# Kernel optimization log

Hardware: AMD Instinct MI355X
Metric: run time of the kernel (lower is better)

The kernel has to match this reference:

```python
import jax, jax.numpy as jnp
import numpy as np

TEMPERATURE = 0.1
GAMMA = 0.5
LOSS_WEIGHT = 1.0
N, D = 8192, 64
EPS_COS = 1e-8
EPS_NCE = 1e-6
SQ_EPS = 1e-12  # (1e-6 distance)^2


def setup_inputs() -> dict:
    key = jax.random.key(0)
    k1, k2, k3 = jax.random.split(key, 3)
    features = jax.random.normal(k1, (N, D), dtype=jnp.float32)
    labels = jax.random.randint(k2, (N,), 0, 3, dtype=jnp.int64)
    coords = jax.random.uniform(k3, (N, 3), dtype=jnp.float32)
    return {"features": features, "labels": labels, "coords": coords}


def reference(features, labels, coords):
    # line-point mask (label == 2); pairwise math on the masked subset is
    # expressed as full pairwise + (m_i & m_j) masking, mathematically
    # identical to extract-then-pairwise in the torch original.
    m = labels == 2                       # [N] bool
    mf = m.astype(features.dtype)
    L = jnp.sum(mf)                       # number of line points

    # cosine similarity: normalize then GEMM (== F.cosine_similarity pairwise)
    norm = jnp.maximum(jnp.linalg.norm(features, axis=1, keepdims=True), EPS_COS)
    fn = features / norm
    feat_sim = fn @ fn.T                  # [N, N]

    # squared pairwise coordinate distances (cdist^2), clamped >= 0
    sq_norm = jnp.sum(coords * coords, axis=1)
    sq = sq_norm[:, None] + sq_norm[None, :] - 2.0 * (coords @ coords.T)
    sq = jnp.maximum(sq, 0.0)             # [N, N]

    pair = m[:, None] & m[None, :]
    within = (sq < 1.0) & (sq > SQ_EPS)   # dist < 1.0 and dist > 1e-6
    pos = pair & within
    neg = pair & ~within                  # original neg_mask = ~pos over subset

    posf = pos.astype(feat_sim.dtype)
    negf = neg.astype(feat_sim.dtype)

    exp_sim = jnp.exp(feat_sim / TEMPERATURE)
    sum_exp = jnp.sum(exp_sim * negf, axis=1)
    pos_sum = jnp.sum(exp_sim * posf, axis=1)
    ratio = pos_sum / (sum_exp + pos_sum + EPS_NCE)
    # mean of -log(ratio) over line points only (guard non-line rows)
    per_point = -jnp.log(jnp.where(m, ratio, 1.0))
    info_nce = jnp.sum(per_point * mf) / L

    # continuity: mean over the L x L subset matrix of |(1 - sim) - dist| * pos
    safe_sq = jnp.where(pos, sq, 1.0)     # avoid sqrt(0) NaN grads on masked entries
    coord_dist = jnp.sqrt(safe_sq)
    continuity = jnp.sum(jnp.abs((1.0 - feat_sim) - coord_dist) * posf) / (L * L)

    return (info_nce + GAMMA * continuity) * LOSS_WEIGHT
```

## Files before the change

### kernel.cpp

```cpp
#include <hip/hip_runtime.h>
#include <math.h>


typedef short s16x8 __attribute__((ext_vector_type(8)));
typedef float f32x4 __attribute__((ext_vector_type(4)));

#define NPTS 8192
#define DIM 64
#define BT 128
#define GRID_P 512
#define PSTRIDE 4096
#define MAXSLOT 32

#define OFF_L 0
#define OFF_IDX 1024
#define OFF_FH (OFF_IDX + NPTS * 4)
#define OFF_FL (OFF_FH + NPTS * DIM * 2)
#define OFF_CS (OFF_FL + NPTS * DIM * 2)
#define OFF_DF (OFF_CS + NPTS * 16)
#define OFF_PP (OFF_DF + NPTS * 4)
#define OFF_PN (OFF_PP + MAXSLOT * PSTRIDE * 4)
#define OFF_CT (OFF_PN + MAXSLOT * PSTRIDE * 4)

__global__ __launch_bounds__(1024) void k_scan(const int* __restrict__ labels,
                                               int* __restrict__ idx,
                                               int* __restrict__ Lout) {
  __shared__ int wres[16];
  __shared__ int wsum[16];
  const int t = threadIdx.x;
  const int lane = t & 63;
  const int wid = t >> 6;
  const int base = t * 8;
  int w[8];
#pragma unroll
  for (int j = 0; j < 8; j++) w[j] = labels[base + j];
  int oddz = (w[1] == 0) && (w[3] == 0) && (w[5] == 0) && (w[7] == 0);
  unsigned long long wa = __ballot(!oddz);
  if (lane == 0) wres[wid] = (wa == 0ull);
  __syncthreads();
  int is64 = 1;
#pragma unroll
  for (int i = 0; i < 16; i++) is64 &= wres[i];

  int bits = 0, cnt = 0;
  if (is64) {
    const long long* l64 = (const long long*)labels;
#pragma unroll
    for (int j = 0; j < 8; j++) {
      bool f = (l64[base + j] == 2ll);
      bits |= ((int)f) << j;
      cnt += (int)f;
    }
  } else {
#pragma unroll
    for (int j = 0; j < 8; j++) {
      bool f = (w[j] == 2);
      bits |= ((int)f) << j;
      cnt += (int)f;
    }
  }
  int inc = cnt;
#pragma unroll
  for (int m = 1; m < 64; m <<= 1) {
    int v = __shfl_up(inc, m);
    if (lane >= m) inc += v;
  }
  if (lane == 63) wsum[wid] = inc;
  __syncthreads();
  if (t < 16) {
    int v = wsum[t];
    int sc = v;
#pragma unroll
    for (int m = 1; m < 16; m <<= 1) {
      int u = __shfl_up(sc, m);
      if (t >= m) sc += u;
    }
    wsum[t] = sc - v;
    if (t == 15) *Lout = sc;
  }
  __syncthreads();
  int pos = wsum[wid] + inc - cnt;
#pragma unroll
  for (int j = 0; j < 8; j++) {
    if (bits & (1 << j)) idx[pos++] = base + j;
  }
}

__global__ __launch_bounds__(256) void k_gather(const float* __restrict__ feats,
                                                const float* __restrict__ coords,
                                                const int* __restrict__ idx,
                                                const int* __restrict__ Lp,
                                                ushort* __restrict__ fnHi,
                                                ushort* __restrict__ fnLo,
                                                float4* __restrict__ cs,
                                                int* __restrict__ diagf) {
  const int L = *Lp;
  const int gw = (int)((blockIdx.x * blockDim.x + threadIdx.x) >> 6);
  const int lane = threadIdx.x & 63;
  if (gw >= L) {
    fnHi[gw * 64 + lane] = 0;
    fnLo[gw * 64 + lane] = 0;
    return;
  }
  const int row = idx[gw];
  float f = feats[row * DIM + lane];
  float ss = f * f;
#pragma unroll
  for (int m = 32; m; m >>= 1) ss += __shfl_xor(ss, m);
  float nrm = fmaxf(sqrtf(ss), 1e-8f);
  float fn = f / nrm;
  unsigned int u = __float_as_uint(fn);
  unsigned int hb = (u + 0x7FFFu + ((u >> 16) & 1u)) >> 16;
  float hif = __uint_as_float(hb << 16);
  float lof = fn - hif;
  unsigned int ul = __float_as_uint(lof);
  unsigned int lb = (ul + 0x7FFFu + ((ul >> 16) & 1u)) >> 16;
  fnHi[gw * 64 + lane] = (ushort)hb;
  fnLo[gw * 64 + lane] = (ushort)lb;
  if (lane == 0) {
    float c0 = coords[row * 3 + 0];
    float c1 = coords[row * 3 + 1];
    float c2 = coords[row * 3 + 2];
    float p0 = __fmul_rn(c0, c0);
    float p1 = __fmul_rn(c1, c1);
    float p2 = __fmul_rn(c2, c2);
    float s = __fadd_rn(__fadd_rn(p0, p1), p2);
    float g = __fadd_rn(__fadd_rn(p0, p2), p1);
    diagf[gw] = (__fadd_rn(s, -g) > 5e-13f) ? 1 : 0;
    cs[gw] = make_float4(c0, c1, c2, c0 * c0 + c1 * c1 + c2 * c2);
  }
}

__global__ __launch_bounds__(256, 2) void k_pair(const ushort* __restrict__ fnHi,
                                                 const ushort* __restrict__ fnLo,
                                                 const float4* __restrict__ cs,
                                                 const int* __restrict__ Lp,
                                                 const int* __restrict__ diagf,
                                                 float* __restrict__ pp,
                                                 float* __restrict__ pn,
                                                 float* __restrict__ contp) {
  __shared__ ushort AB[4][128][72];
  __shared__ float cred[4];

  const int L = *Lp;
  const int nT = (L + BT - 1) >> 7;
  const int nItems = nT * nT;
  const int t = threadIdx.x;
  const int lane = t & 63, wid = t >> 6;
  const int m = lane & 15;
  const int koct = lane >> 4;
  float cont = 0.f;

  for (int wi = blockIdx.x; wi < nItems; wi += GRID_P) {
    const int bi = wi / nT;
    const int jt = wi - bi * nT;
    const int rb = bi << 7, cb = jt << 7;

    __syncthreads();
#pragma unroll
    for (int i = 0; i < 16; i++) {
      int q = t + 256 * i;
      int sel = q >> 10;
      int row = (q >> 3) & 127;
      int oct = q & 7;
      int slot = ((sel < 2) ? rb : cb) + row;
      const ushort* src = (sel & 1) ? fnLo : fnHi;
      s16x8 v = *(const s16x8*)&src[slot * 64 + oct * 8];
      *(s16x8*)&AB[sel][row][oct * 8] = v;
    }
    __syncthreads();

    f32x4 acc[2][8];
#pragma unroll
    for (int rt = 0; rt < 2; rt++)
#pragma unroll
      for (int ct = 0; ct < 8; ct++) acc[rt][ct] = (f32x4){0.f, 0.f, 0.f, 0.f};

#pragma unroll
    for (int kk = 0; kk < 2; kk++) {
      const int kof = kk * 32 + koct * 8;
      s16x8 ah[2], al[2], bh[8], bl[8];
#pragma unroll
      for (int rt = 0; rt < 2; rt++) {
        ah[rt] = *(const s16x8*)&AB[0][wid * 32 + rt * 16 + m][kof];
        al[rt] = *(const s16x8*)&AB[1][wid * 32 + rt * 16 + m][kof];
      }
#pragma unroll
      for (int ct = 0; ct < 8; ct++) {
        bh[ct] = *(const s16x8*)&AB[2][ct * 16 + m][kof];
        bl[ct] = *(const s16x8*)&AB[3][ct * 16 + m][kof];
      }
#pragma unroll
      for (int rt = 0; rt < 2; rt++)
#pragma unroll
        for (int ct = 0; ct < 8; ct++) {
          acc[rt][ct] = __builtin_amdgcn_mfma_f32_16x16x32_bf16(ah[rt], bh[ct], acc[rt][ct], 0, 0, 0);
          acc[rt][ct] = __builtin_amdgcn_mfma_f32_16x16x32_bf16(ah[rt], bl[ct], acc[rt][ct], 0, 0, 0);
          acc[rt][ct] = __builtin_amdgcn_mfma_f32_16x16x32_bf16(al[rt], bh[ct], acc[rt][ct], 0, 0, 0);
        }
    }

    float4 crow[2][4];
    int dfr[2][4];
#pragma unroll
    for (int rt = 0; rt < 2; rt++)
#pragma unroll
      for (int rg = 0; rg < 4; rg++) {
        int ig = rb + wid * 32 + rt * 16 + koct * 4 + rg;
        crow[rt][rg] = cs[ig];
        dfr[rt][rg] = diagf[ig];
      }
    float pos_r[2][4] = {{0.f, 0.f, 0.f, 0.f}, {0.f, 0.f, 0.f, 0.f}};
    float neg_r[2][4] = {{0.f, 0.f, 0.f, 0.f}, {0.f, 0.f, 0.f, 0.f}};
#pragma unroll
    for (int ct = 0; ct < 8; ct++) {
      int jg = cb + ct * 16 + m;
      float4 cbv = cs[jg];
      bool jv = (jg < L);
#pragma unroll
      for (int rt = 0; rt < 2; rt++)
#pragma unroll
        for (int rg = 0; rg < 4; rg++) {
          int ig = rb + wid * 32 + rt * 16 + koct * 4 + rg;
          bool valid = jv && (ig < L);
          float sim = acc[rt][ct][rg];
          float4 cav = crow[rt][rg];
          float d3 = cav.x * cbv.x + cav.y * cbv.y + cav.z * cbv.z;
          float sq = fmaxf(cav.w + cbv.w - 2.f * d3, 0.f);
          bool within = (sq < 1.0f) && (sq > 1e-12f);
          if (ig == jg) within = (dfr[rt][rg] != 0);
          float e = __expf(sim * 10.f);
          if (valid) {
            if (within) {
              pos_r[rt][rg] += e;
              cont += fabsf(1.f - sim - sqrtf(sq));
            } else {
              neg_r[rt][rg] += e;
            }
          }
        }
    }
#pragma unroll
    for (int rt = 0; rt < 2; rt++)
#pragma unroll
      for (int rg = 0; rg < 4; rg++) {
        float p = pos_r[rt][rg], n = neg_r[rt][rg];
#pragma unroll
        for (int s = 1; s < 16; s <<= 1) {
          p += __shfl_xor(p, s);
          n += __shfl_xor(n, s);
        }
        if (m == 0) {
          int ig = rb + wid * 32 + rt * 16 + koct * 4 + rg;
          pp[jt * PSTRIDE + ig] = p;
          pn[jt * PSTRIDE + ig] = n;
        }
      }
  }

#pragma unroll
  for (int s = 1; s < 64; s <<= 1) cont += __shfl_xor(cont, s);
  if (lane == 0) cred[wid] = cont;
  __syncthreads();
  if (t == 0) contp[blockIdx.x] = cred[0] + cred[1] + cred[2] + cred[3];
}

__global__ __launch_bounds__(1024) void k_final(const float* __restrict__ pp,
                                                const float* __restrict__ pn,
                                                const float* __restrict__ contp,
                                                const int* __restrict__ Lp,
                                                float* __restrict__ out) {
  __shared__ float red[32];
  const int L = *Lp;
  const int nslots = (L + BT - 1) >> 7;
  const int t = threadIdx.x;
  float accI = 0.f;
  for (int s = t; s < L; s += 1024) {
    float pos = 0.f, neg = 0.f;
    for (int c = 0; c < nslots; c++) {
      pos += pp[c * PSTRIDE + s];
      neg += pn[c * PSTRIDE + s];
    }
    accI += -logf(pos / (neg + pos + 1e-6f));
  }
  float accC = 0.f;
  for (int c = t; c < GRID_P; c += 1024) accC += contp[c];
#pragma unroll
  for (int m = 1; m < 64; m <<= 1) {
    accI += __shfl_xor(accI, m);
    accC += __shfl_xor(accC, m);
  }
  if ((t & 63) == 0) {
    red[t >> 6] = accI;
    red[16 + (t >> 6)] = accC;
  }
  __syncthreads();
  if (t == 0) {
    float sI = 0.f, sC = 0.f;
#pragma unroll
    for (int w = 0; w < 16; w++) {
      sI += red[w];
      sC += red[16 + w];
    }
    float fL = (float)L;
    out[0] = sI / fL + 0.5f * (sC / (fL * fL));
  }
}

extern "C" void kernel_launch(void* const* d_in, const int* in_sizes, int n_in,
                              void* d_out, int out_size, void* d_ws, size_t ws_size,
                              hipStream_t stream) {
  const float* features = (const float*)d_in[0];
  const int* labels = (const int*)d_in[1];
  const float* coords = (const float*)d_in[2];

  char* ws = (char*)d_ws;
  int* Lp = (int*)(ws + OFF_L);
  int* idx = (int*)(ws + OFF_IDX);
  ushort* fnHi = (ushort*)(ws + OFF_FH);
  ushort* fnLo = (ushort*)(ws + OFF_FL);
  float4* cs = (float4*)(ws + OFF_CS);
  int* diagf = (int*)(ws + OFF_DF);
  float* pp = (float*)(ws + OFF_PP);
  float* pn = (float*)(ws + OFF_PN);
  float* contp = (float*)(ws + OFF_CT);
  float* out = (float*)d_out;

  k_scan<<<1, 1024, 0, stream>>>(labels, idx, Lp);
  k_gather<<<(NPTS * 64) / 256, 256, 0, stream>>>(features, coords, idx, Lp, fnHi, fnLo, cs, diagf);
  k_pair<<<GRID_P, 256, 0, stream>>>(fnHi, fnLo, cs, Lp, diagf, pp, pn, contp);
  k_final<<<1, 1024, 0, stream>>>(pp, pn, contp, Lp, out);
}
```

Measured before the change: 47.94 us.

## Fuse four kernels into one persistent kernel with software grid barriers

Replaces the scan, gather, pair and final kernels with a single persistent kernel of 256 blocks that separates the phases with atomic-counter grid barriers, reset by a memset before launch. The pair stage now stages K in two halves into smaller shared tiles, and the final reduction is spread across blocks. The aim is to remove the launch gaps between the four kernels and the serial single-block final pass. In exchange it adds spin-wait barriers that rely on all 256 blocks being co-resident, an extra memset launch, and fewer blocks for the pair phase.

Measured after the change: 162.7 us. 3.39x slower.

```diff
diff --git a/kernel.cpp b/kernel.cpp
--- a/kernel.cpp
+++ b/kernel.cpp
@@ -7,12 +7,13 @@
 
 #define NPTS 8192
 #define DIM 64
-#define BT 128
-#define GRID_P 512
+#define GRID 256
+#define NTHR 256
 #define PSTRIDE 4096
 #define MAXSLOT 32
 
-#define OFF_L 0
+#define OFF_CNT 0
+#define OFF_L 64
 #define OFF_IDX 1024
 #define OFF_FH (OFF_IDX + NPTS * 4)
 #define OFF_FL (OFF_FH + NPTS * DIM * 2)
@@ -21,289 +22,289 @@
 #define OFF_PP (OFF_DF + NPTS * 4)
 #define OFF_PN (OFF_PP + MAXSLOT * PSTRIDE * 4)
 #define OFF_CT (OFF_PN + MAXSLOT * PSTRIDE * 4)
-
-__global__ __launch_bounds__(1024) void k_scan(const int* __restrict__ labels,
-                                               int* __restrict__ idx,
-                                               int* __restrict__ Lout) {
-  __shared__ int wres[16];
-  __shared__ int wsum[16];
-  const int t = threadIdx.x;
-  const int lane = t & 63;
-  const int wid = t >> 6;
-  const int base = t * 8;
-  int w[8];
-#pragma unroll
-  for (int j = 0; j < 8; j++) w[j] = labels[base + j];
-  int oddz = (w[1] == 0) && (w[3] == 0) && (w[5] == 0) && (w[7] == 0);
-  unsigned long long wa = __ballot(!oddz);
-  if (lane == 0) wres[wid] = (wa == 0ull);
+#define OFF_PI (OFF_CT + GRID * 4)
+
+__device__ __forceinline__ void grid_bar(int* cnt, int target) {
   __syncthreads();
-  int is64 = 1;
-#pragma unroll
-  for (int i = 0; i < 16; i++) is64 &= wres[i];
-
-  int bits = 0, cnt = 0;
-  if (is64) {
-    const long long* l64 = (const long long*)labels;
-#pragma unroll
-    for (int j = 0; j < 8; j++) {
-      bool f = (l64[base + j] == 2ll);
-      bits |= ((int)f) << j;
-      cnt += (int)f;
-    }
-  } else {
-#pragma unroll
-    for (int j = 0; j < 8; j++) {
-      bool f = (w[j] == 2);
-      bits |= ((int)f) << j;
-      cnt += (int)f;
-    }
-  }
-  int inc = cnt;
-#pragma unroll
-  for (int m = 1; m < 64; m <<= 1) {
-    int v = __shfl_up(inc, m);
-    if (lane >= m) inc += v;
-  }
-  if (lane == 63) wsum[wid] = inc;
+  if (threadIdx.x == 0) {
+    __threadfence();
+    atomicAdd(cnt, 1);
+    while (__hip_atomic_load(cnt, __ATOMIC_ACQUIRE, __HIP_MEMORY_SCOPE_AGENT) <
+           target) {
+      __builtin_amdgcn_s_sleep(2);
+    }
+    __threadfence();
+  }
   __syncthreads();
-  if (t < 16) {
-    int v = wsum[t];
-    int sc = v;
-#pragma unroll
-    for (int m = 1; m < 16; m <<= 1) {
-      int u = __shfl_up(sc, m);
-      if (t >= m) sc += u;
-    }
-    wsum[t] = sc - v;
-    if (t == 15) *Lout = sc;
-  }
-  __syncthreads();
-  int pos = wsum[wid] + inc - cnt;
-#pragma unroll
-  for (int j = 0; j < 8; j++) {
-    if (bits & (1 << j)) idx[pos++] = base + j;
-  }
 }
 
-__global__ __launch_bounds__(256) void k_gather(const float* __restrict__ feats,
-                                                const float* __restrict__ coords,
-                                                const int* __restrict__ idx,
-                                                const int* __restrict__ Lp,
-                                                ushort* __restrict__ fnHi,
-                                                ushort* __restrict__ fnLo,
-                                                float4* __restrict__ cs,
-                                                int* __restrict__ diagf) {
-  const int L = *Lp;
-  const int gw = (int)((blockIdx.x * blockDim.x + threadIdx.x) >> 6);
-  const int lane = threadIdx.x & 63;
-  if (gw >= L) {
-    fnHi[gw * 64 + lane] = 0;
-    fnLo[gw * 64 + lane] = 0;
-    return;
-  }
-  const int row = idx[gw];
-  float f = feats[row * DIM + lane];
-  float ss = f * f;
-#pragma unroll
-  for (int m = 32; m; m >>= 1) ss += __shfl_xor(ss, m);
-  float nrm = fmaxf(sqrtf(ss), 1e-8f);
-  float fn = f / nrm;
-  unsigned int u = __float_as_uint(fn);
-  unsigned int hb = (u + 0x7FFFu + ((u >> 16) & 1u)) >> 16;
-  float hif = __uint_as_float(hb << 16);
-  float lof = fn - hif;
-  unsigned int ul = __float_as_uint(lof);
-  unsigned int lb = (ul + 0x7FFFu + ((ul >> 16) & 1u)) >> 16;
-  fnHi[gw * 64 + lane] = (ushort)hb;
-  fnLo[gw * 64 + lane] = (ushort)lb;
-  if (lane == 0) {
-    float c0 = coords[row * 3 + 0];
-    float c1 = coords[row * 3 + 1];
-    float c2 = coords[row * 3 + 2];
-    float p0 = __fmul_rn(c0, c0);
-    float p1 = __fmul_rn(c1, c1);
-    float p2 = __fmul_rn(c2, c2);
-    float s = __fadd_rn(__fadd_rn(p0, p1), p2);
-    float g = __fadd_rn(__fadd_rn(p0, p2), p1);
-    diagf[gw] = (__fadd_rn(s, -g) > 5e-13f) ? 1 : 0;
-    cs[gw] = make_float4(c0, c1, c2, c0 * c0 + c1 * c1 + c2 * c2);
-  }
-}
-
-__global__ __launch_bounds__(256, 2) void k_pair(const ushort* __restrict__ fnHi,
-                                                 const ushort* __restrict__ fnLo,
-                                                 const float4* __restrict__ cs,
-                                                 const int* __restrict__ Lp,
-                                                 const int* __restrict__ diagf,
-                                                 float* __restrict__ pp,
-                                                 float* __restrict__ pn,
-                                                 float* __restrict__ contp) {
-  __shared__ ushort AB[4][128][72];
-  __shared__ float cred[4];
-
-  const int L = *Lp;
-  const int nT = (L + BT - 1) >> 7;
-  const int nItems = nT * nT;
+__global__ __launch_bounds__(NTHR) void k_fused(
+    const float* __restrict__ feats, const int* __restrict__ labels,
+    const float* __restrict__ coords, int* cnt, int* __restrict__ Lp,
+    int* __restrict__ idx, ushort* __restrict__ fnHi,
+    ushort* __restrict__ fnLo, float4* __restrict__ cs,
+    int* __restrict__ diagf, float* __restrict__ pp, float* __restrict__ pn,
+    float* __restrict__ contp, float* __restrict__ partI,
+    float* __restrict__ out) {
+  __shared__ __attribute__((aligned(16))) ushort AB[4][128][40];
+  __shared__ float fred[8];
+  __shared__ int ired[8];
   const int t = threadIdx.x;
   const int lane = t & 63, wid = t >> 6;
-  const int m = lane & 15;
-  const int koct = lane >> 4;
-  float cont = 0.f;
-
-  for (int wi = blockIdx.x; wi < nItems; wi += GRID_P) {
-    const int bi = wi / nT;
-    const int jt = wi - bi * nT;
-    const int rb = bi << 7, cb = jt << 7;
-
-    __syncthreads();
-#pragma unroll
-    for (int i = 0; i < 16; i++) {
-      int q = t + 256 * i;
-      int sel = q >> 10;
-      int row = (q >> 3) & 127;
-      int oct = q & 7;
-      int slot = ((sel < 2) ? rb : cb) + row;
-      const ushort* src = (sel & 1) ? fnLo : fnHi;
-      s16x8 v = *(const s16x8*)&src[slot * 64 + oct * 8];
-      *(s16x8*)&AB[sel][row][oct * 8] = v;
-    }
-    __syncthreads();
-
-    f32x4 acc[2][8];
-#pragma unroll
-    for (int rt = 0; rt < 2; rt++)
-#pragma unroll
-      for (int ct = 0; ct < 8; ct++) acc[rt][ct] = (f32x4){0.f, 0.f, 0.f, 0.f};
-
-#pragma unroll
-    for (int kk = 0; kk < 2; kk++) {
-      const int kof = kk * 32 + koct * 8;
-      s16x8 ah[2], al[2], bh[8], bl[8];
-#pragma unroll
-      for (int rt = 0; rt < 2; rt++) {
-        ah[rt] = *(const s16x8*)&AB[0][wid * 32 + rt * 16 + m][kof];
-        al[rt] = *(const s16x8*)&AB[1][wid * 32 + rt * 16 + m][kof];
-      }
-#pragma unroll
-      for (int ct = 0; ct < 8; ct++) {
-        bh[ct] = *(const s16x8*)&AB[2][ct * 16 + m][kof];
-        bl[ct] = *(const s16x8*)&AB[3][ct * 16 + m][kof];
-      }
+  const int bx = (int)blockIdx.x;
+
+  if (bx == 0) {
+    const int base = t * 32;
+    int w[32];
+#pragma unroll
+    for (int j = 0; j < 32; j++) w[j] = labels[base + j];
+    int oddz = 1;
+#pragma unroll
+    for (int j = 1; j < 32; j += 2) oddz &= (w[j] == 0);
+    unsigned long long wa = __ballot(!oddz);
+    if (lane == 0) ired[wid] = (wa == 0ull);
+    __syncthreads();
+    int is64 = ired[0] & ired[1] & ired[2] & ired[3];
+    __syncthreads();
+    unsigned bits = 0;
+    int cnt2 = 0;
+    if (is64) {
+      const long long* l64 = (const long long*)labels;
+#pragma unroll
+      for (int j = 0; j < 32; j++) {
+        bool f = (l64[base + j] == 2ll);
+        bits |= ((unsigned)f) << j;
+        cnt2 += (int)f;
+      }
+    } else {
+#pragma unroll
+      for (int j = 0; j < 32; j++) {
+        bool f = (w[j] == 2);
+        bits |= ((unsigned)f) << j;
+        cnt2 += (int)f;
+      }
+    }
+    int inc = cnt2;
+#pragma unroll
+    for (int m1 = 1; m1 < 64; m1 <<= 1) {
+      int v = __shfl_up(inc, m1);
+      if (lane >= m1) inc += v;
+    }
+    if (lane == 63) ired[wid] = inc;
+    __syncthreads();
+    int woff = 0;
+#pragma unroll
+    for (int i = 0; i < 4; i++)
+      if (i < wid) woff += ired[i];
+    int pos = woff + inc - cnt2;
+#pragma unroll
+    for (int j = 0; j < 32; j++)
+      if ((bits >> j) & 1u) idx[pos++] = base + j;
+    if (t == 0) *Lp = ired[0] + ired[1] + ired[2] + ired[3];
+  }
+  grid_bar(cnt, GRID);
+
+  const int L = *Lp;
+  const int Lpad = (L + 127) & ~127;
+  const int nT = Lpad >> 7;
+
+  for (int slot = bx * 4 + wid; slot < Lpad; slot += GRID * 4) {
+    if (slot < L) {
+      const int row = idx[slot];
+      float f = feats[row * DIM + lane];
+      float ss = f * f;
+#pragma unroll
+      for (int m1 = 32; m1; m1 >>= 1) ss += __shfl_xor(ss, m1);
+      float nrm = fmaxf(sqrtf(ss), 1e-8f);
+      float fn = f / nrm;
+      unsigned u = __float_as_uint(fn);
+      unsigned hb = (u + 0x7FFFu + ((u >> 16) & 1u)) >> 16;
+      float hif = __uint_as_float(hb << 16);
+      float lof = fn - hif;
+      unsigned ul = __float_as_uint(lof);
+      unsigned lb = (ul + 0x7FFFu + ((ul >> 16) & 1u)) >> 16;
+      fnHi[slot * 64 + lane] = (ushort)hb;
+      fnLo[slot * 64 + lane] = (ushort)lb;
+      if (lane == 0) {
+        float c0 = coords[row * 3 + 0];
+        float c1 = coords[row * 3 + 1];
+        float c2 = coords[row * 3 + 2];
+        float p0 = __fmul_rn(c0, c0);
+        float p1 = __fmul_rn(c1, c1);
+        float p2 = __fmul_rn(c2, c2);
+        float s_ = __fadd_rn(__fadd_rn(p0, p1), p2);
+        float g_ = __fadd_rn(__fadd_rn(p0, p2), p1);
+        diagf[slot] = (__fadd_rn(s_, -g_) > 5e-13f) ? 1 : 0;
+        cs[slot] = make_float4(c0, c1, c2, c0 * c0 + c1 * c1 + c2 * c2);
+      }
+    } else {
+      fnHi[slot * 64 + lane] = 0;
+      fnLo[slot * 64 + lane] = 0;
+      if (lane == 0) {
+        cs[slot] = make_float4(0.f, 0.f, 0.f, 0.f);
+        diagf[slot] = 0;
+      }
+    }
+  }
+  grid_bar(cnt, 2 * GRID);
+
+  {
+    const int nItems = nT * nT;
+    const int m = lane & 15;
+    const int koct = lane >> 4;
+    float cont = 0.f;
+
+    for (int wi = bx; wi < nItems; wi += GRID) {
+      const int bi = wi / nT;
+      const int jt = wi - bi * nT;
+      const int rb = bi << 7, cb = jt << 7;
+
+      f32x4 acc[2][8];
 #pragma unroll
       for (int rt = 0; rt < 2; rt++)
 #pragma unroll
+        for (int ct = 0; ct < 8; ct++) acc[rt][ct] = (f32x4){0.f, 0.f, 0.f, 0.f};
+
+#pragma unroll
+      for (int kk = 0; kk < 2; kk++) {
+        __syncthreads();
+#pragma unroll
+        for (int i = 0; i < 8; i++) {
+          int q = t + 256 * i;
+          int sel = q >> 9;
+          int row = (q >> 2) & 127;
+          int oct = q & 3;
+          int slot = ((sel < 2) ? rb : cb) + row;
+          const ushort* src = (sel & 1) ? fnLo : fnHi;
+          s16x8 v = *(const s16x8*)&src[slot * 64 + kk * 32 + oct * 8];
+          *(s16x8*)&AB[sel][row][oct * 8] = v;
+        }
+        __syncthreads();
+
+        const int kofd = koct * 8;
+        s16x8 ah[2], al[2], bh[8], bl[8];
+#pragma unroll
+        for (int rt = 0; rt < 2; rt++) {
+          ah[rt] = *(const s16x8*)&AB[0][wid * 32 + rt * 16 + m][kofd];
+          al[rt] = *(const s16x8*)&AB[1][wid * 32 + rt * 16 + m][kofd];
+        }
+#pragma unroll
         for (int ct = 0; ct < 8; ct++) {
-          acc[rt][ct] = __builtin_amdgcn_mfma_f32_16x16x32_bf16(ah[rt], bh[ct], acc[rt][ct], 0, 0, 0);
-          acc[rt][ct] = __builtin_amdgcn_mfma_f32_16x16x32_bf16(ah[rt], bl[ct], acc[rt][ct], 0, 0, 0);
-          acc[rt][ct] = __builtin_amdgcn_mfma_f32_16x16x32_bf16(al[rt], bh[ct], acc[rt][ct], 0, 0, 0);
-        }
-    }
-
-    float4 crow[2][4];
-    int dfr[2][4];
-#pragma unroll
-    for (int rt = 0; rt < 2; rt++)
-#pragma unroll
-      for (int rg = 0; rg < 4; rg++) {
-        int ig = rb + wid * 32 + rt * 16 + koct * 4 + rg;
-        crow[rt][rg] = cs[ig];
-        dfr[rt][rg] = diagf[ig];
-      }
-    float pos_r[2][4] = {{0.f, 0.f, 0.f, 0.f}, {0.f, 0.f, 0.f, 0.f}};
-    float neg_r[2][4] = {{0.f, 0.f, 0.f, 0.f}, {0.f, 0.f, 0.f, 0.f}};
-#pragma unroll
-    for (int ct = 0; ct < 8; ct++) {
-      int jg = cb + ct * 16 + m;
-      float4 cbv = cs[jg];
-      bool jv = (jg < L);
+          bh[ct] = *(const s16x8*)&AB[2][ct * 16 + m][kofd];
+          bl[ct] = *(const s16x8*)&AB[3][ct * 16 + m][kofd];
+        }
+#pragma unroll
+        for (int rt = 0; rt < 2; rt++)
+#pragma unroll
+          for (int ct = 0; ct < 8; ct++) {
+            acc[rt][ct] = __builtin_amdgcn_mfma_f32_16x16x32_bf16(ah[rt], bh[ct], acc[rt][ct], 0, 0, 0);
+            acc[rt][ct] = __builtin_amdgcn_mfma_f32_16x16x32_bf16(ah[rt], bl[ct], acc[rt][ct], 0, 0, 0);
+            acc[rt][ct] = __builtin_amdgcn_mfma_f32_16x16x32_bf16(al[rt], bh[ct], acc[rt][ct], 0, 0, 0);
+          }
+      }
+
+      float4 crow[2][4];
+      int dfr[2][4];
 #pragma unroll
       for (int rt = 0; rt < 2; rt++)
 #pragma unroll
         for (int rg = 0; rg < 4; rg++) {
           int ig = rb + wid * 32 + rt * 16 + koct * 4 + rg;
-          bool valid = jv && (ig < L);
-          float sim = acc[rt][ct][rg];
-          float4 cav = crow[rt][rg];
-          float d3 = cav.x * cbv.x + cav.y * cbv.y + cav.z * cbv.z;
-          float sq = fmaxf(cav.w + cbv.w - 2.f * d3, 0.f);
-          bool within = (sq < 1.0f) && (sq > 1e-12f);
-          if (ig == jg) within = (dfr[rt][rg] != 0);
-          float e = __expf(sim * 10.f);
-          if (valid) {
-            if (within) {
-              pos_r[rt][rg] += e;
-              cont += fabsf(1.f - sim - sqrtf(sq));
-            } else {
-              neg_r[rt][rg] += e;
+          crow[rt][rg] = cs[ig];
+          dfr[rt][rg] = diagf[ig];
+        }
+      float pos_r[2][4] = {{0.f, 0.f, 0.f, 0.f}, {0.f, 0.f, 0.f, 0.f}};
+      float neg_r[2][4] = {{0.f, 0.f, 0.f, 0.f}, {0.f, 0.f, 0.f, 0.f}};
+#pragma unroll
+      for (int ct = 0; ct < 8; ct++) {
+        int jg = cb + ct * 16 + m;
+        float4 cbv = cs[jg];
+        bool jv = (jg < L);
+#pragma unroll
+        for (int rt = 0; rt < 2; rt++)
+#pragma unroll
+          for (int rg = 0; rg < 4; rg++) {
+            int ig = rb + wid * 32 + rt * 16 + koct * 4 + rg;
+            bool valid = jv && (ig < L);
+            float sim = acc[rt][ct][rg];
+            float4 cav = crow[rt][rg];
+            float d3 = cav.x * cbv.x + cav.y * cbv.y + cav.z * cbv.z;
+            float sq = fmaxf(cav.w + cbv.w - 2.f * d3, 0.f);
+            bool within = (sq < 1.0f) && (sq > 1e-12f);
+            if (ig == jg) within = (dfr[rt][rg] != 0);
+            float e = __expf(sim * 10.f);
+            if (valid) {
+              if (within) {
+                pos_r[rt][rg] += e;
+                cont += fabsf(1.f - sim - sqrtf(sq));
+              } else {
+                neg_r[rt][rg] += e;
+              }
             }
           }
-        }
-    }
-#pragma unroll
-    for (int rt = 0; rt < 2; rt++)
-#pragma unroll
-      for (int rg = 0; rg < 4; rg++) {
-        float p = pos_r[rt][rg], n = neg_r[rt][rg];
-#pragma unroll
-        for (int s = 1; s < 16; s <<= 1) {
-          p += __shfl_xor(p, s);
-          n += __shfl_xor(n, s);
-        }
-        if (m == 0) {
-          int ig = rb + wid * 32 + rt * 16 + koct * 4 + rg;
-          pp[jt * PSTRIDE + ig] = p;
-          pn[jt * PSTRIDE + ig] = n;
-        }
-      }
-  }
-
-#pragma unroll
-  for (int s = 1; s < 64; s <<= 1) cont += __shfl_xor(cont, s);
-  if (lane == 0) cred[wid] = cont;
-  __syncthreads();
-  if (t == 0) contp[blockIdx.x] = cred[0] + cred[1] + cred[2] + cred[3];
-}
-
-__global__ __launch_bounds__(1024) void k_final(const float* __restrict__ pp,
-                                                const float* __restrict__ pn,
-                                                const float* __restrict__ contp,
-                                                const int* __restrict__ Lp,
-                                                float* __restrict__ out) {
-  __shared__ float red[32];
-  const int L = *Lp;
-  const int nslots = (L + BT - 1) >> 7;
-  const int t = threadIdx.x;
-  float accI = 0.f;
-  for (int s = t; s < L; s += 1024) {
-    float pos = 0.f, neg = 0.f;
-    for (int c = 0; c < nslots; c++) {
-      pos += pp[c * PSTRIDE + s];
-      neg += pn[c * PSTRIDE + s];
-    }
-    accI += -logf(pos / (neg + pos + 1e-6f));
-  }
-  float accC = 0.f;
-  for (int c = t; c < GRID_P; c += 1024) accC += contp[c];
-#pragma unroll
-  for (int m = 1; m < 64; m <<= 1) {
-    accI += __shfl_xor(accI, m);
-    accC += __shfl_xor(accC, m);
-  }
-  if ((t & 63) == 0) {
-    red[t >> 6] = accI;
-    red[16 + (t >> 6)] = accC;
-  }
-  __syncthreads();
-  if (t == 0) {
-    float sI = 0.f, sC = 0.f;
-#pragma unroll
-    for (int w = 0; w < 16; w++) {
-      sI += red[w];
-      sC += red[16 + w];
-    }
-    float fL = (float)L;
-    out[0] = sI / fL + 0.5f * (sC / (fL * fL));
+      }
+#pragma unroll
+      for (int rt = 0; rt < 2; rt++)
+#pragma unroll
+        for (int rg = 0; rg < 4; rg++) {
+          float p = pos_r[rt][rg], n = neg_r[rt][rg];
+#pragma unroll
+          for (int s1 = 1; s1 < 16; s1 <<= 1) {
+            p += __shfl_xor(p, s1);
+            n += __shfl_xor(n, s1);
+          }
+          if (m == 0) {
+            int ig = rb + wid * 32 + rt * 16 + koct * 4 + rg;
+            pp[jt * PSTRIDE + ig] = p;
+            pn[jt * PSTRIDE + ig] = n;
+          }
+        }
+    }
+
+#pragma unroll
+    for (int s1 = 1; s1 < 64; s1 <<= 1) cont += __shfl_xor(cont, s1);
+    __syncthreads();
+    if (lane == 0) fred[wid] = cont;
+    __syncthreads();
+    if (t == 0) contp[bx] = fred[0] + fred[1] + fred[2] + fred[3];
+  }
+  grid_bar(cnt, 3 * GRID);
+
+  const int nRB = (L + NTHR - 1) >> 8;
+  if (bx < nRB) {
+    int s1 = bx * NTHR + t;
+    float aI = 0.f;
+    if (s1 < L) {
+      float pos = 0.f, neg = 0.f;
+      for (int c = 0; c < nT; c++) {
+        pos += pp[c * PSTRIDE + s1];
+        neg += pn[c * PSTRIDE + s1];
+      }
+      aI = -logf(pos / (neg + pos + 1e-6f));
+    }
+#pragma unroll
+    for (int m1 = 1; m1 < 64; m1 <<= 1) aI += __shfl_xor(aI, m1);
+    __syncthreads();
+    if (lane == 0) fred[wid] = aI;
+    __syncthreads();
+    if (t == 0) partI[bx] = fred[0] + fred[1] + fred[2] + fred[3];
+  }
+  grid_bar(cnt, 4 * GRID);
+
+  if (bx == 0) {
+    float c2 = contp[t];
+#pragma unroll
+    for (int m1 = 1; m1 < 64; m1 <<= 1) c2 += __shfl_xor(c2, m1);
+    __syncthreads();
+    if (lane == 0) fred[4 + wid] = c2;
+    __syncthreads();
+    if (t == 0) {
+      float sI = 0.f;
+      for (int b = 0; b < nRB; b++) sI += partI[b];
+      float sC = fred[4] + fred[5] + fred[6] + fred[7];
+      float fL = (float)L;
+      out[0] = sI / fL + 0.5f * (sC / (fL * fL));
+    }
   }
 }
 
@@ -315,6 +316,7 @@
   const float* coords = (const float*)d_in[2];
 
   char* ws = (char*)d_ws;
+  int* cnt = (int*)(ws + OFF_CNT);
   int* Lp = (int*)(ws + OFF_L);
   int* idx = (int*)(ws + OFF_IDX);
   ushort* fnHi = (ushort*)(ws + OFF_FH);
@@ -324,10 +326,11 @@
   float* pp = (float*)(ws + OFF_PP);
   float* pn = (float*)(ws + OFF_PN);
   float* contp = (float*)(ws + OFF_CT);
+  float* partI = (float*)(ws + OFF_PI);
   float* out = (float*)d_out;
 
-  k_scan<<<1, 1024, 0, stream>>>(labels, idx, Lp);
-  k_gather<<<(NPTS * 64) / 256, 256, 0, stream>>>(features, coords, idx, Lp, fnHi, fnLo, cs, diagf);
-  k_pair<<<GRID_P, 256, 0, stream>>>(fnHi, fnLo, cs, Lp, diagf, pp, pn, contp);
-  k_final<<<1, 1024, 0, stream>>>(pp, pn, contp, Lp, out);
+  hipMemsetAsync(cnt, 0, 4, stream);
+  k_fused<<<GRID, NTHR, 0, stream>>>(features, labels, coords, cnt, Lp, idx,
+                                     fnHi, fnLo, cs, diagf, pp, pn, contp,
+                                     partI, out);
 }
```

## Exploit symmetry of pairwise matrix by computing only upper-triangular tiles

Applied to the files above, without the earlier changes.

Iterates only over upper-triangular 128x128 tile pairs. Off-diagonal tiles also produce column-wise positive and negative exp sums, reduced through shared memory and written to the transposed partial slot, and their continuity contribution is weighted by two. This roughly halves the MFMA and exp work. In exchange it adds a linear search for the tile index, an extra shared-memory reduction and barrier per off-diagonal tile, and more registers. The gather kernel now zero-fills the padding coordinates and diagonal flags so the padded columns read defined values.

Measured after the change: 52.59 us. 1.1x slower.

```diff
diff --git a/kernel.cpp b/kernel.cpp
--- a/kernel.cpp
+++ b/kernel.cpp
@@ -100,6 +100,10 @@
   if (gw >= L) {
     fnHi[gw * 64 + lane] = 0;
     fnLo[gw * 64 + lane] = 0;
+    if (lane == 0) {
+      cs[gw] = make_float4(0.f, 0.f, 0.f, 0.f);
+      diagf[gw] = 0;
+    }
     return;
   }
   const int row = idx[gw];
@@ -109,12 +113,12 @@
   for (int m = 32; m; m >>= 1) ss += __shfl_xor(ss, m);
   float nrm = fmaxf(sqrtf(ss), 1e-8f);
   float fn = f / nrm;
-  unsigned int u = __float_as_uint(fn);
-  unsigned int hb = (u + 0x7FFFu + ((u >> 16) & 1u)) >> 16;
+  unsigned u = __float_as_uint(fn);
+  unsigned hb = (u + 0x7FFFu + ((u >> 16) & 1u)) >> 16;
   float hif = __uint_as_float(hb << 16);
   float lof = fn - hif;
-  unsigned int ul = __float_as_uint(lof);
-  unsigned int lb = (ul + 0x7FFFu + ((ul >> 16) & 1u)) >> 16;
+  unsigned ul = __float_as_uint(lof);
+  unsigned lb = (ul + 0x7FFFu + ((ul >> 16) & 1u)) >> 16;
   fnHi[gw * 64 + lane] = (ushort)hb;
   fnLo[gw * 64 + lane] = (ushort)lb;
   if (lane == 0) {
@@ -140,11 +144,13 @@
                                                  float* __restrict__ pn,
                                                  float* __restrict__ contp) {
   __shared__ ushort AB[4][128][72];
+  __shared__ float cscrP[4][8][16];
+  __shared__ float cscrN[4][8][16];
   __shared__ float cred[4];
 
   const int L = *Lp;
   const int nT = (L + BT - 1) >> 7;
-  const int nItems = nT * nT;
+  const int nItems = (nT * (nT + 1)) >> 1;
   const int t = threadIdx.x;
   const int lane = t & 63, wid = t >> 6;
   const int m = lane & 15;
@@ -152,8 +158,14 @@
   float cont = 0.f;
 
   for (int wi = blockIdx.x; wi < nItems; wi += GRID_P) {
-    const int bi = wi / nT;
-    const int jt = wi - bi * nT;
+    int bi = 0, off = 0;
+    while (wi >= off + (nT - bi)) {
+      off += nT - bi;
+      bi++;
+    }
+    const int jt = bi + (wi - off);
+    const bool isOff = (jt != bi);
+    const float scw = isOff ? 2.f : 1.f;
     const int rb = bi << 7, cb = jt << 7;
 
     __syncthreads();
@@ -212,6 +224,8 @@
       }
     float pos_r[2][4] = {{0.f, 0.f, 0.f, 0.f}, {0.f, 0.f, 0.f, 0.f}};
     float neg_r[2][4] = {{0.f, 0.f, 0.f, 0.f}, {0.f, 0.f, 0.f, 0.f}};
+    float colP[8] = {0.f, 0.f, 0.f, 0.f, 0.f, 0.f, 0.f, 0.f};
+    float colN[8] = {0.f, 0.f, 0.f, 0.f, 0.f, 0.f, 0.f, 0.f};
 #pragma unroll
     for (int ct = 0; ct < 8; ct++) {
       int jg = cb + ct * 16 + m;
@@ -233,10 +247,16 @@
           if (valid) {
             if (within) {
               pos_r[rt][rg] += e;
-              cont += fabsf(1.f - sim - sqrtf(sq));
+              cont += scw * fabsf(1.f - sim - sqrtf(sq));
             } else {
               neg_r[rt][rg] += e;
             }
+            if (isOff) {
+              if (within)
+                colP[ct] += e;
+              else
+                colN[ct] += e;
+            }
           }
         }
     }
@@ -246,9 +266,9 @@
       for (int rg = 0; rg < 4; rg++) {
         float p = pos_r[rt][rg], n = neg_r[rt][rg];
 #pragma unroll
-        for (int s = 1; s < 16; s <<= 1) {
-          p += __shfl_xor(p, s);
-          n += __shfl_xor(n, s);
+        for (int s1 = 1; s1 < 16; s1 <<= 1) {
+          p += __shfl_xor(p, s1);
+          n += __shfl_xor(n, s1);
         }
         if (m == 0) {
           int ig = rb + wid * 32 + rt * 16 + koct * 4 + rg;
@@ -256,10 +276,36 @@
           pn[jt * PSTRIDE + ig] = n;
         }
       }
-  }
-
-#pragma unroll
-  for (int s = 1; s < 64; s <<= 1) cont += __shfl_xor(cont, s);
+    if (isOff) {
+#pragma unroll
+      for (int ct = 0; ct < 8; ct++) {
+        float p = colP[ct], n = colN[ct];
+        p += __shfl_xor(p, 16);
+        p += __shfl_xor(p, 32);
+        n += __shfl_xor(n, 16);
+        n += __shfl_xor(n, 32);
+        if (lane < 16) {
+          cscrP[wid][ct][lane] = p;
+          cscrN[wid][ct][lane] = n;
+        }
+      }
+      __syncthreads();
+      if (t < 128) {
+        int c2 = t >> 4, m2 = t & 15;
+        float P = cscrP[0][c2][m2] + cscrP[1][c2][m2] + cscrP[2][c2][m2] +
+                  cscrP[3][c2][m2];
+        float N = cscrN[0][c2][m2] + cscrN[1][c2][m2] + cscrN[2][c2][m2] +
+                  cscrN[3][c2][m2];
+        int jg = cb + c2 * 16 + m2;
+        pp[bi * PSTRIDE + jg] = P;
+        pn[bi * PSTRIDE + jg] = N;
+      }
+    }
+  }
+
+#pragma unroll
+  for (int s1 = 1; s1 < 64; s1 <<= 1) cont += __shfl_xor(cont, s1);
+  __syncthreads();
   if (lane == 0) cred[wid] = cont;
   __syncthreads();
   if (t == 0) contp[blockIdx.x] = cred[0] + cred[1] + cred[2] + cred[3];
```

## Fuse scan with gather and fold the final reduction into the pair kernel

Applied to the files above, without the earlier changes.

The label scan and the gather/normalize step are merged into one 64-block kernel. Each block redundantly recomputes the compaction scan in shared memory, then handles a strided share of the rows. The final reduction moves into the pair kernel as a last-block-done step using an atomic counter and thread fences, so four launches become two. The trade-off is redundant scan work in every block, a slower barrier-based Hillis-Steele scan, and reliance on fences and the counter for correctness.

Measured after the change: 93.05 us. 94.1% more time.

```diff
diff --git a/kernel.cpp b/kernel.cpp
--- a/kernel.cpp
+++ b/kernel.cpp
@@ -13,8 +13,8 @@
 #define MAXSLOT 32
 
 #define OFF_L 0
-#define OFF_IDX 1024
-#define OFF_FH (OFF_IDX + NPTS * 4)
+#define OFF_DONE 64
+#define OFF_FH 1024
 #define OFF_FL (OFF_FH + NPTS * DIM * 2)
 #define OFF_CS (OFF_FL + NPTS * DIM * 2)
 #define OFF_DF (OFF_CS + NPTS * 16)
@@ -22,15 +22,23 @@
 #define OFF_PN (OFF_PP + MAXSLOT * PSTRIDE * 4)
 #define OFF_CT (OFF_PN + MAXSLOT * PSTRIDE * 4)
 
-__global__ __launch_bounds__(1024) void k_scan(const int* __restrict__ labels,
-                                               int* __restrict__ idx,
-                                               int* __restrict__ Lout) {
+__global__ __launch_bounds__(1024) void k_prep(const float* __restrict__ feats,
+                                               const int* __restrict__ labels,
+                                               const float* __restrict__ coords,
+                                               int* __restrict__ Lp,
+                                               int* __restrict__ done,
+                                               ushort* __restrict__ fnHi,
+                                               ushort* __restrict__ fnLo,
+                                               float4* __restrict__ cs,
+                                               int* __restrict__ diagf) {
+  __shared__ int sc[1024];
+  __shared__ int sidx[NPTS];
   __shared__ int wres[16];
-  __shared__ int wsum[16];
   const int t = threadIdx.x;
   const int lane = t & 63;
   const int wid = t >> 6;
   const int base = t * 8;
+
   int w[8];
 #pragma unroll
   for (int j = 0; j < 8; j++) w[j] = labels[base + j];
@@ -59,75 +67,65 @@
       cnt += (int)f;
     }
   }
-  int inc = cnt;
-#pragma unroll
-  for (int m = 1; m < 64; m <<= 1) {
-    int v = __shfl_up(inc, m);
-    if (lane >= m) inc += v;
-  }
-  if (lane == 63) wsum[wid] = inc;
-  __syncthreads();
-  if (t < 16) {
-    int v = wsum[t];
-    int sc = v;
-#pragma unroll
-    for (int m = 1; m < 16; m <<= 1) {
-      int u = __shfl_up(sc, m);
-      if (t >= m) sc += u;
-    }
-    wsum[t] = sc - v;
-    if (t == 15) *Lout = sc;
-  }
-  __syncthreads();
-  int pos = wsum[wid] + inc - cnt;
+  sc[t] = cnt;
+  __syncthreads();
+  for (int off = 1; off < 1024; off <<= 1) {
+    int v = 0;
+    if (t >= off) v = sc[t - off];
+    __syncthreads();
+    sc[t] += v;
+    __syncthreads();
+  }
+  int pos = sc[t] - cnt;
 #pragma unroll
   for (int j = 0; j < 8; j++) {
-    if (bits & (1 << j)) idx[pos++] = base + j;
-  }
-}
-
-__global__ __launch_bounds__(256) void k_gather(const float* __restrict__ feats,
-                                                const float* __restrict__ coords,
-                                                const int* __restrict__ idx,
-                                                const int* __restrict__ Lp,
-                                                ushort* __restrict__ fnHi,
-                                                ushort* __restrict__ fnLo,
-                                                float4* __restrict__ cs,
-                                                int* __restrict__ diagf) {
-  const int L = *Lp;
-  const int gw = (int)((blockIdx.x * blockDim.x + threadIdx.x) >> 6);
-  const int lane = threadIdx.x & 63;
-  if (gw >= L) {
-    fnHi[gw * 64 + lane] = 0;
-    fnLo[gw * 64 + lane] = 0;
-    return;
-  }
-  const int row = idx[gw];
-  float f = feats[row * DIM + lane];
-  float ss = f * f;
-#pragma unroll
-  for (int m = 32; m; m >>= 1) ss += __shfl_xor(ss, m);
-  float nrm = fmaxf(sqrtf(ss), 1e-8f);
-  float fn = f / nrm;
-  unsigned int u = __float_as_uint(fn);
-  unsigned int hb = (u + 0x7FFFu + ((u >> 16) & 1u)) >> 16;
-  float hif = __uint_as_float(hb << 16);
-  float lof = fn - hif;
-  unsigned int ul = __float_as_uint(lof);
-  unsigned int lb = (ul + 0x7FFFu + ((ul >> 16) & 1u)) >> 16;
-  fnHi[gw * 64 + lane] = (ushort)hb;
-  fnLo[gw * 64 + lane] = (ushort)lb;
-  if (lane == 0) {
-    float c0 = coords[row * 3 + 0];
-    float c1 = coords[row * 3 + 1];
-    float c2 = coords[row * 3 + 2];
-    float p0 = __fmul_rn(c0, c0);
-    float p1 = __fmul_rn(c1, c1);
-    float p2 = __fmul_rn(c2, c2);
-    float s = __fadd_rn(__fadd_rn(p0, p1), p2);
-    float g = __fadd_rn(__fadd_rn(p0, p2), p1);
-    diagf[gw] = (__fadd_rn(s, -g) > 5e-13f) ? 1 : 0;
-    cs[gw] = make_float4(c0, c1, c2, c0 * c0 + c1 * c1 + c2 * c2);
+    if (bits & (1 << j)) sidx[pos++] = base + j;
+  }
+  __syncthreads();
+  const int L = sc[1023];
+  if (blockIdx.x == 0 && t == 0) {
+    *Lp = L;
+    *done = 0;
+  }
+  const int Lpad = (L + 127) & ~127;
+
+  for (int slot = (int)blockIdx.x * 16 + wid; slot < Lpad; slot += 64 * 16) {
+    if (slot < L) {
+      const int row = sidx[slot];
+      float f = feats[row * DIM + lane];
+      float ss = f * f;
+#pragma unroll
+      for (int m1 = 32; m1; m1 >>= 1) ss += __shfl_xor(ss, m1);
+      float nrm = fmaxf(sqrtf(ss), 1e-8f);
+      float fn = f / nrm;
+      unsigned u = __float_as_uint(fn);
+      unsigned hb = (u + 0x7FFFu + ((u >> 16) & 1u)) >> 16;
+      float hif = __uint_as_float(hb << 16);
+      float lof = fn - hif;
+      unsigned ul = __float_as_uint(lof);
+      unsigned lb = (ul + 0x7FFFu + ((ul >> 16) & 1u)) >> 16;
+      fnHi[slot * 64 + lane] = (ushort)hb;
+      fnLo[slot * 64 + lane] = (ushort)lb;
+      if (lane == 0) {
+        float c0 = coords[row * 3 + 0];
+        float c1 = coords[row * 3 + 1];
+        float c2 = coords[row * 3 + 2];
+        float p0 = __fmul_rn(c0, c0);
+        float p1 = __fmul_rn(c1, c1);
+        float p2 = __fmul_rn(c2, c2);
+        float s_ = __fadd_rn(__fadd_rn(p0, p1), p2);
+        float g_ = __fadd_rn(__fadd_rn(p0, p2), p1);
+        diagf[slot] = (__fadd_rn(s_, -g_) > 5e-13f) ? 1 : 0;
+        cs[slot] = make_float4(c0, c1, c2, c0 * c0 + c1 * c1 + c2 * c2);
+      }
+    } else {
+      fnHi[slot * 64 + lane] = 0;
+      fnLo[slot * 64 + lane] = 0;
+      if (lane == 0) {
+        cs[slot] = make_float4(0.f, 0.f, 0.f, 0.f);
+        diagf[slot] = 0;
+      }
+    }
   }
 }
 
@@ -138,9 +136,12 @@
                                                  const int* __restrict__ diagf,
                                                  float* __restrict__ pp,
                                                  float* __restrict__ pn,
-                                                 float* __restrict__ contp) {
+                                                 float* __restrict__ contp,
+                                                 int* __restrict__ done,
+                                                 float* __restrict__ out) {
   __shared__ ushort AB[4][128][72];
-  __shared__ float cred[4];
+  __shared__ float cred[8];
+  __shared__ int lastFlag;
 
   const int L = *Lp;
   const int nT = (L + BT - 1) >> 7;
@@ -246,9 +247,9 @@
       for (int rg = 0; rg < 4; rg++) {
         float p = pos_r[rt][rg], n = neg_r[rt][rg];
 #pragma unroll
-        for (int s = 1; s < 16; s <<= 1) {
-          p += __shfl_xor(p, s);
-          n += __shfl_xor(n, s);
+        for (int s1 = 1; s1 < 16; s1 <<= 1) {
+          p += __shfl_xor(p, s1);
+          n += __shfl_xor(n, s1);
         }
         if (m == 0) {
           int ig = rb + wid * 32 + rt * 16 + koct * 4 + rg;
@@ -259,51 +260,50 @@
   }
 
 #pragma unroll
-  for (int s = 1; s < 64; s <<= 1) cont += __shfl_xor(cont, s);
+  for (int s1 = 1; s1 < 64; s1 <<= 1) cont += __shfl_xor(cont, s1);
+  __syncthreads();
   if (lane == 0) cred[wid] = cont;
   __syncthreads();
   if (t == 0) contp[blockIdx.x] = cred[0] + cred[1] + cred[2] + cred[3];
-}
-
-__global__ __launch_bounds__(1024) void k_final(const float* __restrict__ pp,
-                                                const float* __restrict__ pn,
-                                                const float* __restrict__ contp,
-                                                const int* __restrict__ Lp,
-                                                float* __restrict__ out) {
-  __shared__ float red[32];
-  const int L = *Lp;
-  const int nslots = (L + BT - 1) >> 7;
-  const int t = threadIdx.x;
-  float accI = 0.f;
-  for (int s = t; s < L; s += 1024) {
-    float pos = 0.f, neg = 0.f;
-    for (int c = 0; c < nslots; c++) {
-      pos += pp[c * PSTRIDE + s];
-      neg += pn[c * PSTRIDE + s];
-    }
-    accI += -logf(pos / (neg + pos + 1e-6f));
-  }
-  float accC = 0.f;
-  for (int c = t; c < GRID_P; c += 1024) accC += contp[c];
-#pragma unroll
-  for (int m = 1; m < 64; m <<= 1) {
-    accI += __shfl_xor(accI, m);
-    accC += __shfl_xor(accC, m);
-  }
-  if ((t & 63) == 0) {
-    red[t >> 6] = accI;
-    red[16 + (t >> 6)] = accC;
-  }
+
+  __threadfence();
   __syncthreads();
   if (t == 0) {
-    float sI = 0.f, sC = 0.f;
-#pragma unroll
-    for (int w = 0; w < 16; w++) {
-      sI += red[w];
-      sC += red[16 + w];
-    }
-    float fL = (float)L;
-    out[0] = sI / fL + 0.5f * (sC / (fL * fL));
+    int prev = atomicAdd(done, 1);
+    lastFlag = (prev == GRID_P - 1);
+  }
+  __syncthreads();
+  if (lastFlag) {
+    __threadfence();
+    float accI = 0.f;
+    for (int s = t; s < L; s += 256) {
+      float pos = 0.f, neg = 0.f;
+#pragma unroll 4
+      for (int c = 0; c < nT; c++) {
+        pos += pp[c * PSTRIDE + s];
+        neg += pn[c * PSTRIDE + s];
+      }
+      accI += -logf(pos / (neg + pos + 1e-6f));
+    }
+    float accC = 0.f;
+    for (int c = t; c < GRID_P; c += 256) accC += contp[c];
+#pragma unroll
+    for (int m1 = 1; m1 < 64; m1 <<= 1) {
+      accI += __shfl_xor(accI, m1);
+      accC += __shfl_xor(accC, m1);
+    }
+    __syncthreads();
+    if (lane == 0) {
+      cred[wid] = accI;
+      cred[4 + wid] = accC;
+    }
+    __syncthreads();
+    if (t == 0) {
+      float sI = cred[0] + cred[1] + cred[2] + cred[3];
+      float sC = cred[4] + cred[5] + cred[6] + cred[7];
+      float fL = (float)L;
+      out[0] = sI / fL + 0.5f * (sC / (fL * fL));
+    }
   }
 }
 
@@ -316,7 +316,7 @@
 
   char* ws = (char*)d_ws;
   int* Lp = (int*)(ws + OFF_L);
-  int* idx = (int*)(ws + OFF_IDX);
+  int* done = (int*)(ws + OFF_DONE);
   ushort* fnHi = (ushort*)(ws + OFF_FH);
   ushort* fnLo = (ushort*)(ws + OFF_FL);
   float4* cs = (float4*)(ws + OFF_CS);
@@ -326,8 +326,8 @@
   float* contp = (float*)(ws + OFF_CT);
   float* out = (float*)d_out;
 
-  k_scan<<<1, 1024, 0, stream>>>(labels, idx, Lp);
-  k_gather<<<(NPTS * 64) / 256, 256, 0, stream>>>(features, coords, idx, Lp, fnHi, fnLo, cs, diagf);
-  k_pair<<<GRID_P, 256, 0, stream>>>(fnHi, fnLo, cs, Lp, diagf, pp, pn, contp);
-  k_final<<<1, 1024, 0, stream>>>(pp, pn, contp, Lp, out);
+  k_prep<<<64, 1024, 0, stream>>>(features, labels, coords, Lp, done, fnHi,
+                                  fnLo, cs, diagf);
+  k_pair<<<GRID_P, 256, 0, stream>>>(fnHi, fnLo, cs, Lp, diagf, pp, pn, contp,
+                                     done, out);
 }
```
